# Kernel tuning notes

Hardware: AMD Instinct MI355X
Metric: run time of the kernel (lower is better)

The kernel has to match this reference:

```python
import jax, jax.numpy as jnp
import numpy as np
import math

B, M, V, C, HID, BIN, H, W = 2, 1024, 300, 128, 128, 256, 384, 512


def fibonacci_sphere(n):
    # generate_grasp_views: n approximately-uniform directions on the unit sphere
    i = np.arange(n, dtype=np.float64)
    phi = (np.sqrt(5.0) - 1.0) / 2.0
    z = (2.0 * i + 1.0) / n - 1.0
    r = np.sqrt(np.maximum(1.0 - z * z, 0.0))
    t = 2.0 * np.pi * i * phi
    v = np.stack([r * np.cos(t), r * np.sin(t), z], -1)
    return (v / np.linalg.norm(v, axis=-1, keepdims=True)).astype(np.float32)


def setup_inputs():
    key = jax.random.key(0)
    ks = jax.random.split(key, 24)
    seed_features = jax.random.normal(ks[0], (B, C, M), jnp.float32)
    token_sel_idx = jax.random.randint(ks[1], (B, M), 0, H * W)
    fx = 525.0
    Kmat = jnp.array([[fx, 0.0, W / 2.0], [0.0, fx, H / 2.0], [0.0, 0.0, 1.0]], jnp.float32)
    K = jnp.broadcast_to(Kmat, (B, 3, 3))
    depth_map = 0.2 + 0.8 * jax.random.uniform(ks[2], (B, 1, H, W), jnp.float32)
    depth_prob = jax.nn.softmax(jax.random.normal(ks[3], (B, BIN, H, W), jnp.float32), axis=1)
    view_dirs = jnp.asarray(fibonacci_sphere(V))

    def lin(k, fan_in, shape):
        s = 1.0 / np.sqrt(fan_in)
        return jax.random.uniform(k, shape, jnp.float32, -s, s)

    qin = C + 7  # seed_feat + ray(3) + normal(3) + uncert(1)
    params = dict(
        Wq1=lin(ks[4], qin, (qin, HID)), bq1=lin(ks[5], qin, (HID,)),
        Wq2=lin(ks[6], HID, (HID, HID)), bq2=lin(ks[7], HID, (HID,)),
        Wa1=lin(ks[8], 3, (3, HID)), ba1=lin(ks[9], 3, (HID,)),
        Wa2=lin(ks[10], HID, (HID, HID)), ba2=lin(ks[11], HID, (HID,)),
        Wb1=lin(ks[12], 3, (3, HID // 2)), bb1=lin(ks[13], 3, (HID // 2,)),
        Wb2=lin(ks[14], HID // 2, (HID // 2, 1)), bb2=lin(ks[15], HID // 2, (1,)),
        Wr1=lin(ks[16], HID, (HID, C)), br1=lin(ks[17], HID, (C,)),
        Wr2=lin(ks[18], C, (C, C)), br2=lin(ks[19], C, (C,)),
    )
    return dict(seed_features=seed_features, token_sel_idx=token_sel_idx, K=K,
                depth_map=depth_map, depth_prob=depth_prob, view_dirs=view_dirs, **params)


def _views_to_rot(views):
    # batch_viewpoint_params_to_matrix(-views, angle=0)
    axis_x = -views
    zero = jnp.zeros_like(axis_x[..., 0])
    axis_y = jnp.stack([-axis_x[..., 1], axis_x[..., 0], zero], -1)
    ny = jnp.linalg.norm(axis_y, axis=-1, keepdims=True)
    fallback = jnp.broadcast_to(jnp.array([0.0, 1.0, 0.0], views.dtype), axis_y.shape)
    axis_y = jnp.where(ny < 1e-8, fallback, axis_y / jnp.maximum(ny, 1e-8))
    axis_x = axis_x / jnp.maximum(jnp.linalg.norm(axis_x, axis=-1, keepdims=True), 1e-8)
    axis_z = jnp.cross(axis_x, axis_y)
    return jnp.stack([axis_x, axis_y, axis_z], -1)  # (B,M,3,3)


def _forward(seed_features, token_sel_idx, K, depth_map, depth_prob, view_dirs,
             Wq1, bq1, Wq2, bq2, Wa1, ba1, Wa2, ba2, Wb1, bb1, Wb2, bb2, Wr1, br1, Wr2, br2):
    depth_map = jax.lax.stop_gradient(depth_map)   # .detach() in torch
    depth_prob = jax.lax.stop_gradient(depth_prob)
    # --- backproject depth to xyz map (B,3,H,W) ---
    ys, xs = jnp.meshgrid(jnp.arange(H, dtype=jnp.float32), jnp.arange(W, dtype=jnp.float32), indexing='ij')
    fx = K[:, 0, 0][:, None, None, None]; fy = K[:, 1, 1][:, None, None, None]
    cx = K[:, 0, 2][:, None, None, None]; cy = K[:, 1, 2][:, None, None, None]
    z = depth_map
    x = (xs[None, None] - cx) / fx * z
    y = (ys[None, None] - cy) / fy * z
    xyz = jnp.concatenate([x, y, z], axis=1)
    # --- central-difference normal map with replicate pad ---
    dx = (xyz[:, :, :, 2:] - xyz[:, :, :, :-2])[:, :, 1:-1, :]
    dy = (xyz[:, :, 2:, :] - xyz[:, :, :-2, :])[:, :, :, 1:-1]
    n = jnp.cross(dx.transpose(0, 2, 3, 1), dy.transpose(0, 2, 3, 1))
    n = n / jnp.maximum(jnp.linalg.norm(n, axis=-1, keepdims=True), 1e-6)
    normal_map = jnp.pad(n.transpose(0, 3, 1, 2), ((0, 0), (0, 0), (1, 1), (1, 1)), mode='edge')
    # --- depth uncertainty: normalized entropy over bins ---
    p = jnp.maximum(depth_prob, 1e-8)
    uncert_map = jnp.clip(-(p * jnp.log(p)).sum(axis=1, keepdims=True) / math.log(BIN), 0.0, 1.0)
    # --- per-seed irregular gathers ---
    def gather(feat, idx):
        Bf, Cf = feat.shape[0], feat.shape[1]
        flat = feat.reshape(Bf, Cf, H * W)
        return jnp.take_along_axis(flat, jnp.broadcast_to(idx[:, None, :], (Bf, Cf, idx.shape[1])), axis=2)
    normal_bm3 = gather(normal_map, token_sel_idx).transpose(0, 2, 1)  # (B,M,3)
    uncert_bm1 = gather(uncert_map, token_sel_idx).transpose(0, 2, 1)  # (B,M,1)
    u = (token_sel_idx % W).astype(jnp.float32)
    v = (token_sel_idx // W).astype(jnp.float32)
    rx = (u - K[:, 0, 2][:, None]) / K[:, 0, 0][:, None]
    ry = (v - K[:, 1, 2][:, None]) / K[:, 1, 1][:, None]
    rays = jnp.stack([rx, ry, jnp.ones_like(rx)], -1)
    rays = rays / jnp.maximum(jnp.linalg.norm(rays, axis=-1, keepdims=True), 1e-12)
    normal_bm3 = normal_bm3 * (1.0 - uncert_bm1)
    # --- query / anchor / bias MLPs ---
    q_in = jnp.concatenate([seed_features.transpose(0, 2, 1), rays, normal_bm3, uncert_bm1], -1)
    q = jax.nn.relu(jax.nn.relu(q_in @ Wq1 + bq1) @ Wq2 + bq2)          # (B,M,HID)
    a = jax.nn.relu(view_dirs @ Wa1 + ba1) @ Wa2 + ba2                  # (V,HID)
    bias = (jax.nn.relu(view_dirs @ Wb1 + bb1) @ Wb2 + bb2)[:, 0]        # (V,)
    logits = jnp.einsum('bmh,vh->bmv', q, a) / jnp.sqrt(jnp.float32(HID)) + bias
    view_score = jax.nn.sigmoid(logits)                                  # (B,M,V)
    # --- top-1 view selection + gather xyz / rot / anchor feat ---
    top_inds = jnp.argmax(view_score, axis=-1)                           # (B,M)
    top_xyz = view_dirs[top_inds]                                        # (B,M,3)
    rot = _views_to_rot(top_xyz)                                         # (B,M,3,3)
    top_a = a[top_inds]                                                  # (B,M,HID)
    res = jax.nn.relu((q + top_a) @ Wr1 + br1) @ Wr2 + br2               # (B,M,C)
    res_feat = res.transpose(0, 2, 1)                                    # (B,C,M)
    return view_score, top_inds, top_xyz, rot, res_feat


def reference(seed_features, token_sel_idx, K, depth_map, depth_prob, view_dirs,
              Wq1, bq1, Wq2, bq2, Wa1, ba1, Wa2, ba2, Wb1, bb1, Wb2, bb2, Wr1, br1, Wr2, br2):
    return _forward(seed_features, token_sel_idx, K, depth_map, depth_prob, view_dirs,
                    Wq1, bq1, Wq2, bq2, Wa1, ba1, Wa2, ba2, Wb1, bb1, Wb2, bb2, Wr1, br1, Wr2, br2)
```

## Files before the change

### kernel.cpp

```cpp
#include <hip/hip_runtime.h>
#include <math.h>

#define B 2
#define M 1024
#define V 300
#define C 128
#define HID 128
#define BIN 256
#define H 384
#define W 512
#define QIN (C + 7)

__global__ __launch_bounds__(128) void transpose_seed(
    const float* __restrict__ in, float* __restrict__ out) {
  __shared__ float tile[32][33];
  const int b  = blockIdx.z;
  const int c0 = blockIdx.x * 32;
  const int m0 = blockIdx.y * 32;
  const int tx = threadIdx.x;
#pragma unroll
  for (int r = threadIdx.y; r < 32; r += 4)
    tile[r][tx] = in[((size_t)b * C + c0 + r) * M + m0 + tx];
  __syncthreads();
#pragma unroll
  for (int r = threadIdx.y; r < 32; r += 4)
    out[((size_t)b * M + m0 + r) * C + c0 + tx] = tile[tx][r];
}

__global__ __launch_bounds__(HID) void anchor_kernel(
    const float* __restrict__ view_dirs,
    const float* __restrict__ Wa1, const float* __restrict__ ba1,
    const float* __restrict__ Wa2, const float* __restrict__ ba2,
    const float* __restrict__ Wb1, const float* __restrict__ bb1,
    const float* __restrict__ Wb2, const float* __restrict__ bb2,
    float* __restrict__ a_out, float* __restrict__ aT_out,
    float* __restrict__ bias_out) {
  const int v = blockIdx.x;
  const int t = threadIdx.x;
  __shared__ float h1[HID];

  const float vd0 = view_dirs[v * 3 + 0];
  const float vd1 = view_dirs[v * 3 + 1];
  const float vd2 = view_dirs[v * 3 + 2];

  float h = vd0 * Wa1[0 * HID + t] + vd1 * Wa1[1 * HID + t] + vd2 * Wa1[2 * HID + t] + ba1[t];
  h1[t] = fmaxf(h, 0.0f);

  if (t < 64) {
    float x = vd0 * Wb1[0 * 64 + t] + vd1 * Wb1[1 * 64 + t] + vd2 * Wb1[2 * 64 + t] + bb1[t];
    x = fmaxf(x, 0.0f) * Wb2[t];
#pragma unroll
    for (int o = 32; o > 0; o >>= 1) x += __shfl_down(x, o, 64);
    if (t == 0) bias_out[v] = x + bb2[0];
  }
  __syncthreads();

  float acc = ba2[t];
#pragma unroll 8
  for (int k = 0; k < HID; ++k) acc += h1[k] * Wa2[k * HID + t];
  a_out[v * HID + t] = acc;
  aT_out[(size_t)t * V + v] = acc;
}

__global__ __launch_bounds__(128) void seed_kernel(
    const float* __restrict__ seedT, const int* __restrict__ token_sel_idx,
    const float* __restrict__ Kmat, const float* __restrict__ depth_map,
    const float* __restrict__ depth_prob, const float* __restrict__ view_dirs,
    const float* __restrict__ Wq1, const float* __restrict__ bq1,
    const float* __restrict__ Wq2, const float* __restrict__ bq2,
    const float* __restrict__ Wr1, const float* __restrict__ br1,
    const float* __restrict__ Wr2, const float* __restrict__ br2,
    const float* __restrict__ a_ws, const float* __restrict__ aT_ws,
    const float* __restrict__ bias_ws,
    float* __restrict__ out_view_score, float* __restrict__ out_top_inds,
    float* __restrict__ out_top_xyz, float* __restrict__ out_rot,
    float* __restrict__ out_res) {
  const int bm = blockIdx.x;
  const int b = bm / M;
  const int m = bm - b * M;
  const int t = threadIdx.x;
  const int lane = t & 63;
  const int wv = t >> 6;

  __shared__ float qin_s[QIN + 1];
  __shared__ float hs[HID];
  __shared__ float qs[HID];
  __shared__ float atop_s[HID];
  __shared__ float ered[2];
  __shared__ float wbv[2];
  __shared__ int   wbi[2];
  __shared__ int   sbest;

  qin_s[t] = seedT[((size_t)b * M + m) * C + t];

  const int idx = token_sel_idx[b * M + m];

  {
    const float* dp = depth_prob + (size_t)b * BIN * H * W + idx;
    float p0 = fmaxf(dp[(size_t)(2 * t + 0) * (H * W)], 1e-8f);
    float p1 = fmaxf(dp[(size_t)(2 * t + 1) * (H * W)], 1e-8f);
    float e = p0 * logf(p0) + p1 * logf(p1);
#pragma unroll
    for (int o = 32; o > 0; o >>= 1) e += __shfl_down(e, o, 64);
    if (lane == 0) ered[wv] = e;
  }
  __syncthreads();

  if (t == 0) {
    float uncert = (-(ered[0] + ered[1])) / 5.5451774444795623f;
    uncert = fminf(fmaxf(uncert, 0.0f), 1.0f);

    const float fx = Kmat[b * 9 + 0], fy = Kmat[b * 9 + 4];
    const float cx = Kmat[b * 9 + 2], cy = Kmat[b * 9 + 5];
    const int w = idx % W;
    const int h = idx / W;
    const int hc = min(max(h, 1), H - 2);
    const int wc = min(max(w, 1), W - 2);

    const float* dm = depth_map + (size_t)b * H * W;
    const float zl = dm[hc * W + (wc - 1)];
    const float zr = dm[hc * W + (wc + 1)];
    const float zu = dm[(hc - 1) * W + wc];
    const float zd = dm[(hc + 1) * W + wc];

    const float dxx = (wc + 1 - cx) / fx * zr - (wc - 1 - cx) / fx * zl;
    const float dxy = (hc - cy) / fy * zr - (hc - cy) / fy * zl;
    const float dxz = zr - zl;
    const float dyx = (wc - cx) / fx * zd - (wc - cx) / fx * zu;
    const float dyy = (hc + 1 - cy) / fy * zd - (hc - 1 - cy) / fy * zu;
    const float dyz = zd - zu;

    float nx = dxy * dyz - dxz * dyy;
    float ny = dxz * dyx - dxx * dyz;
    float nz = dxx * dyy - dxy * dyx;
    const float nn = fmaxf(sqrtf(nx * nx + ny * ny + nz * nz), 1e-6f);
    const float sc = (1.0f - uncert) / nn;

    const float rx = ((float)w - cx) / fx;
    const float ry = ((float)h - cy) / fy;
    const float rn = fmaxf(sqrtf(rx * rx + ry * ry + 1.0f), 1e-12f);

    qin_s[128] = rx / rn;
    qin_s[129] = ry / rn;
    qin_s[130] = 1.0f / rn;
    qin_s[131] = nx * sc;
    qin_s[132] = ny * sc;
    qin_s[133] = nz * sc;
    qin_s[134] = uncert;
  }
  __syncthreads();

  float acc = bq1[t];
#pragma unroll 5
  for (int i = 0; i < QIN; ++i) acc += qin_s[i] * Wq1[i * HID + t];
  hs[t] = fmaxf(acc, 0.0f);
  __syncthreads();

  acc = bq2[t];
#pragma unroll 8
  for (int k = 0; k < HID; ++k) acc += hs[k] * Wq2[k * HID + t];
  qs[t] = fmaxf(acc, 0.0f);
  __syncthreads();

  const int col2 = 256 + (t < 44 ? t : 43);
  float d0 = 0.0f, d1 = 0.0f, d2 = 0.0f;
#pragma unroll 8
  for (int k = 0; k < HID; ++k) {
    const float qk = qs[k];
    const float* row = aT_ws + (size_t)k * V;
    d0 += qk * row[t];
    d1 += qk * row[t + 128];
    d2 += qk * row[col2];
  }
  const float rsq = 0.08838834764831845f;
  const float sc0 = 1.0f / (1.0f + expf(-(d0 * rsq + bias_ws[t])));
  const float sc1 = 1.0f / (1.0f + expf(-(d1 * rsq + bias_ws[t + 128])));
  const float sc2 = 1.0f / (1.0f + expf(-(d2 * rsq + bias_ws[col2])));

  float* vs_out = out_view_score + (size_t)bm * V;
  vs_out[t] = sc0;
  vs_out[t + 128] = sc1;
  if (t < 44) vs_out[t + 256] = sc2;

  float bv = sc0; int bi = t;
  if (sc1 > bv) { bv = sc1; bi = t + 128; }
  if (t < 44 && sc2 > bv) { bv = sc2; bi = t + 256; }
#pragma unroll
  for (int o = 32; o > 0; o >>= 1) {
    const float ov = __shfl_down(bv, o, 64);
    const int oi = __shfl_down(bi, o, 64);
    if (ov > bv || (ov == bv && oi < bi)) { bv = ov; bi = oi; }
  }
  if (lane == 0) { wbv[wv] = bv; wbi[wv] = bi; }
  __syncthreads();

  if (t == 0) {
    float fbv = wbv[0]; int fbi = wbi[0];
    if (wbv[1] > fbv || (wbv[1] == fbv && wbi[1] < fbi)) { fbv = wbv[1]; fbi = wbi[1]; }
    sbest = fbi;

    out_top_inds[bm] = (float)fbi;
    const float vx = view_dirs[fbi * 3 + 0];
    const float vy = view_dirs[fbi * 3 + 1];
    const float vz = view_dirs[fbi * 3 + 2];
    out_top_xyz[(size_t)bm * 3 + 0] = vx;
    out_top_xyz[(size_t)bm * 3 + 1] = vy;
    out_top_xyz[(size_t)bm * 3 + 2] = vz;

    float ax0 = -vx, ax1 = -vy, ax2 = -vz;
    float ay0 = vy, ay1 = -vx, ay2 = 0.0f;
    const float nyn = sqrtf(ay0 * ay0 + ay1 * ay1);
    if (nyn < 1e-8f) {
      ay0 = 0.0f; ay1 = 1.0f; ay2 = 0.0f;
    } else {
      const float d = fmaxf(nyn, 1e-8f);
      ay0 /= d; ay1 /= d;
    }
    const float an = fmaxf(sqrtf(ax0 * ax0 + ax1 * ax1 + ax2 * ax2), 1e-8f);
    ax0 /= an; ax1 /= an; ax2 /= an;
    const float az0 = ax1 * ay2 - ax2 * ay1;
    const float az1 = ax2 * ay0 - ax0 * ay2;
    const float az2 = ax0 * ay1 - ax1 * ay0;
    float* R = out_rot + (size_t)bm * 9;
    R[0] = ax0; R[1] = ay0; R[2] = az0;
    R[3] = ax1; R[4] = ay1; R[5] = az1;
    R[6] = ax2; R[7] = ay2; R[8] = az2;
  }
  __syncthreads();
  const int best = sbest;

  atop_s[t] = a_ws[best * HID + t];
  __syncthreads();

  float racc = br1[t];
#pragma unroll 8
  for (int k = 0; k < HID; ++k) racc += (qs[k] + atop_s[k]) * Wr1[k * HID + t];
  hs[t] = fmaxf(racc, 0.0f);
  __syncthreads();

  racc = br2[t];
#pragma unroll 8
  for (int k = 0; k < HID; ++k) racc += hs[k] * Wr2[k * HID + t];
  out_res[((size_t)b * C + t) * M + m] = racc;
}

extern "C" void kernel_launch(void* const* d_in, const int* in_sizes, int n_in,
                              void* d_out, int out_size, void* d_ws, size_t ws_size,
                              hipStream_t stream) {
  const float* seed  = (const float*)d_in[0];
  const int*   tok   = (const int*)d_in[1];
  const float* Km    = (const float*)d_in[2];
  const float* dmap  = (const float*)d_in[3];
  const float* dprob = (const float*)d_in[4];
  const float* vdirs = (const float*)d_in[5];
  const float* Wq1 = (const float*)d_in[6];  const float* bq1 = (const float*)d_in[7];
  const float* Wq2 = (const float*)d_in[8];  const float* bq2 = (const float*)d_in[9];
  const float* Wa1 = (const float*)d_in[10]; const float* ba1 = (const float*)d_in[11];
  const float* Wa2 = (const float*)d_in[12]; const float* ba2 = (const float*)d_in[13];
  const float* Wb1 = (const float*)d_in[14]; const float* bb1 = (const float*)d_in[15];
  const float* Wb2 = (const float*)d_in[16]; const float* bb2 = (const float*)d_in[17];
  const float* Wr1 = (const float*)d_in[18]; const float* br1 = (const float*)d_in[19];
  const float* Wr2 = (const float*)d_in[20]; const float* br2 = (const float*)d_in[21];

  float* out = (float*)d_out;
  float* vs  = out;
  float* ti  = vs + (size_t)B * M * V;
  float* tx  = ti + (size_t)B * M;
  float* rot = tx + (size_t)B * M * 3;
  float* rf  = rot + (size_t)B * M * 9;

  float* a_ws    = (float*)d_ws;
  float* aT_ws   = a_ws + (size_t)V * HID;
  float* bias_ws = aT_ws + (size_t)HID * V;
  float* seedT   = bias_ws + V;

  transpose_seed<<<dim3(C / 32, M / 32, B), dim3(32, 4), 0, stream>>>(seed, seedT);
  anchor_kernel<<<V, HID, 0, stream>>>(vdirs, Wa1, ba1, Wa2, ba2, Wb1, bb1, Wb2, bb2,
                                       a_ws, aT_ws, bias_ws);
  seed_kernel<<<B * M, 128, 0, stream>>>(seedT, tok, Km, dmap, dprob, vdirs,
                                         Wq1, bq1, Wq2, bq2, Wr1, br1, Wr2, br2,
                                         a_ws, aT_ws, bias_ws, vs, ti, tx, rot, rf);
}
```

Baseline: 550.3 us.

## Process eight seeds per block to reuse weight loads across seeds

The seed kernel now handles eight seed points per 256-thread block instead of one. Each weight element loaded from global memory is reused across four or eight seeds in registers, which cuts weight traffic per seed. The separate transpose kernel is removed; seed features are read directly in strided form into shared memory. The view-score argmax is now a per-seed reduction over shared memory. This uses more shared memory and registers per block, and leaves fewer blocks (256) in the grid.

```diff
diff --git a/kernel.cpp b/kernel.cpp
--- a/kernel.cpp
+++ b/kernel.cpp
@@ -10,22 +10,7 @@
 #define H 384
 #define W 512
 #define QIN (C + 7)
-
-__global__ __launch_bounds__(128) void transpose_seed(
-    const float* __restrict__ in, float* __restrict__ out) {
-  __shared__ float tile[32][33];
-  const int b  = blockIdx.z;
-  const int c0 = blockIdx.x * 32;
-  const int m0 = blockIdx.y * 32;
-  const int tx = threadIdx.x;
-#pragma unroll
-  for (int r = threadIdx.y; r < 32; r += 4)
-    tile[r][tx] = in[((size_t)b * C + c0 + r) * M + m0 + tx];
-  __syncthreads();
-#pragma unroll
-  for (int r = threadIdx.y; r < 32; r += 4)
-    out[((size_t)b * M + m0 + r) * C + c0 + tx] = tile[tx][r];
-}
+#define TM 8
 
 __global__ __launch_bounds__(HID) void anchor_kernel(
     const float* __restrict__ view_dirs,
@@ -62,8 +47,8 @@
   aT_out[(size_t)t * V + v] = acc;
 }
 
-__global__ __launch_bounds__(128) void seed_kernel(
-    const float* __restrict__ seedT, const int* __restrict__ token_sel_idx,
+__global__ __launch_bounds__(256) void seed_kernel(
+    const float* __restrict__ seed_features, const int* __restrict__ token_sel_idx,
     const float* __restrict__ Kmat, const float* __restrict__ depth_map,
     const float* __restrict__ depth_prob, const float* __restrict__ view_dirs,
     const float* __restrict__ Wq1, const float* __restrict__ bq1,
@@ -75,39 +60,50 @@
     float* __restrict__ out_view_score, float* __restrict__ out_top_inds,
     float* __restrict__ out_top_xyz, float* __restrict__ out_rot,
     float* __restrict__ out_res) {
-  const int bm = blockIdx.x;
-  const int b = bm / M;
-  const int m = bm - b * M;
+  const int bm0 = blockIdx.x * TM;
+  const int b = bm0 / M;
+  const int m0 = bm0 - b * M;
   const int t = threadIdx.x;
   const int lane = t & 63;
   const int wv = t >> 6;
 
-  __shared__ float qin_s[QIN + 1];
-  __shared__ float hs[HID];
-  __shared__ float qs[HID];
-  __shared__ float atop_s[HID];
-  __shared__ float ered[2];
-  __shared__ float wbv[2];
-  __shared__ int   wbi[2];
-  __shared__ int   sbest;
-
-  qin_s[t] = seedT[((size_t)b * M + m) * C + t];
-
-  const int idx = token_sel_idx[b * M + m];
-
-  {
-    const float* dp = depth_prob + (size_t)b * BIN * H * W + idx;
-    float p0 = fmaxf(dp[(size_t)(2 * t + 0) * (H * W)], 1e-8f);
-    float p1 = fmaxf(dp[(size_t)(2 * t + 1) * (H * W)], 1e-8f);
-    float e = p0 * logf(p0) + p1 * logf(p1);
-#pragma unroll
-    for (int o = 32; o > 0; o >>= 1) e += __shfl_down(e, o, 64);
-    if (lane == 0) ered[wv] = e;
-  }
-  __syncthreads();
-
-  if (t == 0) {
-    float uncert = (-(ered[0] + ered[1])) / 5.5451774444795623f;
+  __shared__ float qin[TM][QIN + 1];
+  __shared__ float hs[TM][HID];
+  __shared__ float qs[TM][HID];
+  __shared__ float sc_s[TM][304];
+  __shared__ float atop[TM][HID];
+  __shared__ float ered[TM];
+  __shared__ int   sidx[TM];
+  __shared__ int   sbest[TM];
+
+  if (t < TM) sidx[t] = token_sel_idx[bm0 + t];
+
+  for (int i = t; i < TM * C; i += 256) {
+    const int s = i & 7;
+    const int c = i >> 3;
+    qin[s][c] = seed_features[((size_t)b * C + c) * M + m0 + s];
+  }
+  __syncthreads();
+
+  {
+    const int es = t >> 5;
+    const int sub = t & 31;
+    const float* dp = depth_prob + (size_t)b * BIN * H * W + sidx[es];
+    float e = 0.0f;
+#pragma unroll
+    for (int j = 0; j < 8; ++j) {
+      const float p = fmaxf(dp[(size_t)(sub + 32 * j) * (H * W)], 1e-8f);
+      e += p * logf(p);
+    }
+#pragma unroll
+    for (int o = 16; o > 0; o >>= 1) e += __shfl_down(e, o, 32);
+    if (sub == 0) ered[es] = e;
+  }
+  __syncthreads();
+
+  if (t < TM) {
+    const int idx = sidx[t];
+    float uncert = (-ered[t]) / 5.5451774444795623f;
     uncert = fminf(fmaxf(uncert, 0.0f), 1.0f);
 
     const float fx = Kmat[b * 9 + 0], fy = Kmat[b * 9 + 4];
@@ -140,69 +136,97 @@
     const float ry = ((float)h - cy) / fy;
     const float rn = fmaxf(sqrtf(rx * rx + ry * ry + 1.0f), 1e-12f);
 
-    qin_s[128] = rx / rn;
-    qin_s[129] = ry / rn;
-    qin_s[130] = 1.0f / rn;
-    qin_s[131] = nx * sc;
-    qin_s[132] = ny * sc;
-    qin_s[133] = nz * sc;
-    qin_s[134] = uncert;
-  }
-  __syncthreads();
-
-  float acc = bq1[t];
+    qin[t][128] = rx / rn;
+    qin[t][129] = ry / rn;
+    qin[t][130] = 1.0f / rn;
+    qin[t][131] = nx * sc;
+    qin[t][132] = ny * sc;
+    qin[t][133] = nz * sc;
+    qin[t][134] = uncert;
+  }
+  __syncthreads();
+
+  const int col = t & 127;
+  const int grp = (t >> 7) * 4;
+  {
+    float acc0 = bq1[col], acc1 = acc0, acc2 = acc0, acc3 = acc0;
 #pragma unroll 5
-  for (int i = 0; i < QIN; ++i) acc += qin_s[i] * Wq1[i * HID + t];
-  hs[t] = fmaxf(acc, 0.0f);
-  __syncthreads();
-
-  acc = bq2[t];
+    for (int i = 0; i < QIN; ++i) {
+      const float w = Wq1[i * HID + col];
+      acc0 += qin[grp + 0][i] * w;
+      acc1 += qin[grp + 1][i] * w;
+      acc2 += qin[grp + 2][i] * w;
+      acc3 += qin[grp + 3][i] * w;
+    }
+    hs[grp + 0][col] = fmaxf(acc0, 0.0f);
+    hs[grp + 1][col] = fmaxf(acc1, 0.0f);
+    hs[grp + 2][col] = fmaxf(acc2, 0.0f);
+    hs[grp + 3][col] = fmaxf(acc3, 0.0f);
+  }
+  __syncthreads();
+
+  {
+    float acc0 = bq2[col], acc1 = acc0, acc2 = acc0, acc3 = acc0;
 #pragma unroll 8
-  for (int k = 0; k < HID; ++k) acc += hs[k] * Wq2[k * HID + t];
-  qs[t] = fmaxf(acc, 0.0f);
-  __syncthreads();
-
-  const int col2 = 256 + (t < 44 ? t : 43);
-  float d0 = 0.0f, d1 = 0.0f, d2 = 0.0f;
-#pragma unroll 8
-  for (int k = 0; k < HID; ++k) {
-    const float qk = qs[k];
-    const float* row = aT_ws + (size_t)k * V;
-    d0 += qk * row[t];
-    d1 += qk * row[t + 128];
-    d2 += qk * row[col2];
-  }
+    for (int k = 0; k < HID; ++k) {
+      const float w = Wq2[k * HID + col];
+      acc0 += hs[grp + 0][k] * w;
+      acc1 += hs[grp + 1][k] * w;
+      acc2 += hs[grp + 2][k] * w;
+      acc3 += hs[grp + 3][k] * w;
+    }
+    qs[grp + 0][col] = fmaxf(acc0, 0.0f);
+    qs[grp + 1][col] = fmaxf(acc1, 0.0f);
+    qs[grp + 2][col] = fmaxf(acc2, 0.0f);
+    qs[grp + 3][col] = fmaxf(acc3, 0.0f);
+  }
+  __syncthreads();
+
   const float rsq = 0.08838834764831845f;
-  const float sc0 = 1.0f / (1.0f + expf(-(d0 * rsq + bias_ws[t])));
-  const float sc1 = 1.0f / (1.0f + expf(-(d1 * rsq + bias_ws[t + 128])));
-  const float sc2 = 1.0f / (1.0f + expf(-(d2 * rsq + bias_ws[col2])));
-
-  float* vs_out = out_view_score + (size_t)bm * V;
-  vs_out[t] = sc0;
-  vs_out[t + 128] = sc1;
-  if (t < 44) vs_out[t + 256] = sc2;
-
-  float bv = sc0; int bi = t;
-  if (sc1 > bv) { bv = sc1; bi = t + 128; }
-  if (t < 44 && sc2 > bv) { bv = sc2; bi = t + 256; }
-#pragma unroll
-  for (int o = 32; o > 0; o >>= 1) {
-    const float ov = __shfl_down(bv, o, 64);
-    const int oi = __shfl_down(bi, o, 64);
-    if (ov > bv || (ov == bv && oi < bi)) { bv = ov; bi = oi; }
-  }
-  if (lane == 0) { wbv[wv] = bv; wbi[wv] = bi; }
-  __syncthreads();
-
-  if (t == 0) {
-    float fbv = wbv[0]; int fbi = wbi[0];
-    if (wbv[1] > fbv || (wbv[1] == fbv && wbi[1] < fbi)) { fbv = wbv[1]; fbi = wbi[1]; }
-    sbest = fbi;
-
-    out_top_inds[bm] = (float)fbi;
-    const float vx = view_dirs[fbi * 3 + 0];
-    const float vy = view_dirs[fbi * 3 + 1];
-    const float vz = view_dirs[fbi * 3 + 2];
+  for (int v = t; v < V; v += 256) {
+    float d[TM];
+#pragma unroll
+    for (int s = 0; s < TM; ++s) d[s] = 0.0f;
+#pragma unroll 4
+    for (int k = 0; k < HID; ++k) {
+      const float av = aT_ws[(size_t)k * V + v];
+#pragma unroll
+      for (int s = 0; s < TM; ++s) d[s] += qs[s][k] * av;
+    }
+    const float bsv = bias_ws[v];
+#pragma unroll
+    for (int s = 0; s < TM; ++s) {
+      const float scv = 1.0f / (1.0f + expf(-(d[s] * rsq + bsv)));
+      sc_s[s][v] = scv;
+      out_view_score[(size_t)(bm0 + s) * V + v] = scv;
+    }
+  }
+  __syncthreads();
+
+  for (int s = wv; s < TM; s += 4) {
+    float bv = -1.0f;
+    int bi = 0;
+    for (int v = lane; v < V; v += 64) {
+      const float x = sc_s[s][v];
+      if (x > bv) { bv = x; bi = v; }
+    }
+#pragma unroll
+    for (int o = 32; o > 0; o >>= 1) {
+      const float ov = __shfl_down(bv, o, 64);
+      const int oi = __shfl_down(bi, o, 64);
+      if (ov > bv || (ov == bv && oi < bi)) { bv = ov; bi = oi; }
+    }
+    if (lane == 0) sbest[s] = bi;
+  }
+  __syncthreads();
+
+  if (t < TM) {
+    const int best = sbest[t];
+    const int bm = bm0 + t;
+    out_top_inds[bm] = (float)best;
+    const float vx = view_dirs[best * 3 + 0];
+    const float vy = view_dirs[best * 3 + 1];
+    const float vz = view_dirs[best * 3 + 2];
     out_top_xyz[(size_t)bm * 3 + 0] = vx;
     out_top_xyz[(size_t)bm * 3 + 1] = vy;
     out_top_xyz[(size_t)bm * 3 + 2] = vz;
@@ -226,22 +250,44 @@
     R[3] = ax1; R[4] = ay1; R[5] = az1;
     R[6] = ax2; R[7] = ay2; R[8] = az2;
   }
-  __syncthreads();
-  const int best = sbest;
-
-  atop_s[t] = a_ws[best * HID + t];
-  __syncthreads();
-
-  float racc = br1[t];
+
+  for (int i = t; i < TM * HID; i += 256) {
+    const int s = i >> 7;
+    const int k = i & 127;
+    atop[s][k] = a_ws[(size_t)sbest[s] * HID + k];
+  }
+  __syncthreads();
+
+  {
+    float acc0 = br1[col], acc1 = acc0, acc2 = acc0, acc3 = acc0;
 #pragma unroll 8
-  for (int k = 0; k < HID; ++k) racc += (qs[k] + atop_s[k]) * Wr1[k * HID + t];
-  hs[t] = fmaxf(racc, 0.0f);
-  __syncthreads();
-
-  racc = br2[t];
+    for (int k = 0; k < HID; ++k) {
+      const float w = Wr1[k * HID + col];
+      acc0 += (qs[grp + 0][k] + atop[grp + 0][k]) * w;
+      acc1 += (qs[grp + 1][k] + atop[grp + 1][k]) * w;
+      acc2 += (qs[grp + 2][k] + atop[grp + 2][k]) * w;
+      acc3 += (qs[grp + 3][k] + atop[grp + 3][k]) * w;
+    }
+    hs[grp + 0][col] = fmaxf(acc0, 0.0f);
+    hs[grp + 1][col] = fmaxf(acc1, 0.0f);
+    hs[grp + 2][col] = fmaxf(acc2, 0.0f);
+    hs[grp + 3][col] = fmaxf(acc3, 0.0f);
+  }
+  __syncthreads();
+
+  {
+    float acc0 = br2[col], acc1 = acc0, acc2 = acc0, acc3 = acc0;
 #pragma unroll 8
-  for (int k = 0; k < HID; ++k) racc += hs[k] * Wr2[k * HID + t];
-  out_res[((size_t)b * C + t) * M + m] = racc;
+    for (int k = 0; k < HID; ++k) {
+      const float w = Wr2[k * HID + col];
+      acc0 += hs[grp + 0][k] * w;
+      acc1 += hs[grp + 1][k] * w;
+      acc2 += hs[grp + 2][k] * w;
+      acc3 += hs[grp + 3][k] * w;
+    }
+    float* o = out_res + ((size_t)b * C + col) * M + m0 + grp;
+    o[0] = acc0; o[1] = acc1; o[2] = acc2; o[3] = acc3;
+  }
 }
 
 extern "C" void kernel_launch(void* const* d_in, const int* in_sizes, int n_in,
@@ -272,12 +318,10 @@
   float* a_ws    = (float*)d_ws;
   float* aT_ws   = a_ws + (size_t)V * HID;
   float* bias_ws = aT_ws + (size_t)HID * V;
-  float* seedT   = bias_ws + V;
-
-  transpose_seed<<<dim3(C / 32, M / 32, B), dim3(32, 4), 0, stream>>>(seed, seedT);
+
   anchor_kernel<<<V, HID, 0, stream>>>(vdirs, Wa1, ba1, Wa2, ba2, Wb1, bb1, Wb2, bb2,
                                        a_ws, aT_ws, bias_ws);
-  seed_kernel<<<B * M, 128, 0, stream>>>(seedT, tok, Km, dmap, dprob, vdirs,
-                                         Wq1, bq1, Wq2, bq2, Wr1, br1, Wr2, br2,
-                                         a_ws, aT_ws, bias_ws, vs, ti, tx, rot, rf);
+  seed_kernel<<<(B * M) / TM, 256, 0, stream>>>(seed, tok, Km, dmap, dprob, vdirs,
+                                                Wq1, bq1, Wq2, bq2, Wr1, br1, Wr2, br2,
+                                                a_ws, aT_ws, bias_ws, vs, ti, tx, rot, rf);
 }
```

After: 558.4 us. No clear change (+1.5%).
